# Kernel optimization log

Hardware: AMD Instinct MI355X
Metric: run time of the kernel (lower is better)

The kernel has to match this reference:

```python
import jax, jax.numpy as jnp
import numpy as np
import math

B, T, D, H = 4, 2048, 1024, 16
HD = D // H  # head dim = 64

def setup_inputs() -> dict:
    key = jax.random.key(0)
    ks = jax.random.split(key, 4)
    scale = 1.0 / math.sqrt(D)
    return {
        "x": jax.random.normal(ks[0], (B, T, D), dtype=jnp.float32),
        "Wq": jax.random.normal(ks[1], (D, D), dtype=jnp.float32) * scale,
        "bq": jnp.zeros((D,), dtype=jnp.float32),
        "Wk": jax.random.normal(ks[2], (D, D), dtype=jnp.float32) * scale,
        "bk": jnp.zeros((D,), dtype=jnp.float32),
        "Wv": jax.random.normal(ks[3], (D, D), dtype=jnp.float32) * scale,
        "bv": jnp.zeros((D,), dtype=jnp.float32),
    }

def reference(x, Wq, bq, Wk, bk, Wv, bv):
    b, t, d = x.shape
    # QKV projections (nn.Dense): x @ W + b
    q = x @ Wq + bq
    k = x @ Wk + bk
    v = x @ Wv + bv
    # b n (h d) -> b h n d
    def split_heads(y):
        return y.reshape(b, t, H, HD).transpose(0, 2, 1, 3)
    q, k, v = split_heads(q), split_heads(k), split_heads(v)
    # scaled dot-product attention; scale by sqrt(features // heads)
    scores = jnp.einsum("bhqd,bhkd->bhqk", q, k) / math.sqrt(HD)
    attn = jax.nn.softmax(scores, axis=-1)
    # dropout rate 0.0 / eval mode => identity
    out = jnp.einsum("bhqk,bhkd->bhqd", attn, v)
    # b h n d -> b n (h d)
    return out.transpose(0, 2, 1, 3).reshape(b, t, d)
```

## Files before the change

kernel.cpp:

```cpp
#include <hip/hip_runtime.h>
#include <math.h>

typedef unsigned short u16;
typedef short short8 __attribute__((ext_vector_type(8)));
typedef u16 u16x4 __attribute__((ext_vector_type(4)));
typedef float f32x4 __attribute__((ext_vector_type(4)));
typedef __bf16 bf16x8 __attribute__((ext_vector_type(8)));

#define B_ 4
#define T_ 2048
#define D_ 1024
#define H_ 16
#define HD_ 64
#define BT_ 8192

__device__ __forceinline__ u16 f2bf(float f) {
  unsigned u = __builtin_bit_cast(unsigned, f);
  u = u + 0x7fffu + ((u >> 16) & 1u);
  return (u16)(u >> 16);
}
__device__ __forceinline__ f32x4 mfma16(short8 a, short8 b, f32x4 c) {
  return __builtin_amdgcn_mfma_f32_16x16x32_bf16(
      __builtin_bit_cast(bf16x8, a), __builtin_bit_cast(bf16x8, b), c, 0, 0, 0);
}
__device__ __forceinline__ void async16(u16* lds, const u16* g) {
  __builtin_amdgcn_global_load_lds(
      (const __attribute__((address_space(1))) unsigned int*)g,
      (__attribute__((address_space(3))) unsigned int*)lds, 16, 0, 0);
}

__global__ __launch_bounds__(256) void convert_x(const float* __restrict__ in,
                                                 u16* __restrict__ out) {
  int i = (blockIdx.x * 256 + threadIdx.x) * 4;
  float4 v = *(const float4*)&in[i];
  u16x4 o = {f2bf(v.x), f2bf(v.y), f2bf(v.z), f2bf(v.w)};
  *(u16x4*)&out[i] = o;
}

__global__ __launch_bounds__(256) void transposeW3(
    const float* __restrict__ Wq, const float* __restrict__ Wk,
    const float* __restrict__ Wv, u16* __restrict__ wtq, u16* __restrict__ wtk,
    u16* __restrict__ wtv) {
  __shared__ float sh[32][33];
  const int wsel = blockIdx.y >> 5;
  const float* in = (wsel == 0) ? Wq : (wsel == 1) ? Wk : Wv;
  u16* out = (wsel == 0) ? wtq : (wsel == 1) ? wtk : wtv;
  const int bx = blockIdx.x * 32, by = (blockIdx.y & 31) * 32;
  const int col = threadIdx.x & 31, r8 = threadIdx.x >> 5;
#pragma unroll
  for (int i = 0; i < 4; i++) {
    int row = r8 + i * 8;
    sh[row][col] = in[(size_t)(by + row) * 1024 + bx + col];
  }
  __syncthreads();
#pragma unroll
  for (int i = 0; i < 4; i++) {
    int row = r8 + i * 8;
    out[(size_t)(bx + row) * 1024 + by + col] = f2bf(sh[col][row]);
  }
}

__global__ __launch_bounds__(256, 2) void gemm_qkv3(
    const u16* __restrict__ xbf, const u16* __restrict__ wtq,
    const u16* __restrict__ wtk, const u16* __restrict__ wtv,
    const float* __restrict__ bq, const float* __restrict__ bk,
    const float* __restrict__ bv, u16* __restrict__ qh, u16* __restrict__ kh,
    u16* __restrict__ vth, float qscale) {
  __shared__ __align__(16) u16 Rs[2][128 * 64];
  __shared__ __align__(16) u16 Cs[2][128 * 64];
  const int proj = blockIdx.y >> 3;
  const int fy = blockIdx.y & 7;
  const u16* Rm;
  const u16* Cm;
  const float* bias;
  u16* out;
  float scale;
  int r0, c0, vmode;
  if (proj == 0) {
    Rm = wtq; Cm = xbf; bias = bq; out = qh; scale = qscale; vmode = 0;
    r0 = fy * 128; c0 = blockIdx.x * 128;
  } else if (proj == 1) {
    Rm = wtk; Cm = xbf; bias = bk; out = kh; scale = 1.0f; vmode = 0;
    r0 = fy * 128; c0 = blockIdx.x * 128;
  } else {
    Rm = xbf; Cm = wtv; bias = bv; out = vth; scale = 1.0f; vmode = 1;
    r0 = blockIdx.x * 128; c0 = fy * 128;
  }
  const int tid = threadIdx.x;
  const int lane = tid & 63;
  const int w = tid >> 6;
  const int wr = w >> 1, wc = w & 1;
  const int c = lane & 15, q4 = lane >> 4;
  const int cx7 = c & 7;

  f32x4 acc[4][4];
#pragma unroll
  for (int i = 0; i < 4; i++)
#pragma unroll
    for (int j = 0; j < 4; j++) {
      f32x4 z = {0.f, 0.f, 0.f, 0.f};
      acc[i][j] = z;
    }

  const int sr = tid >> 3, pc = tid & 7;

#pragma unroll
  for (int i = 0; i < 4; i++) {
    int row = i * 32 + sr;
    int sc = (pc ^ (row & 7)) * 8;
    async16(&Rs[0][(i * 256 + tid) * 8], &Rm[(size_t)(r0 + row) * 1024 + sc]);
    async16(&Cs[0][(i * 256 + tid) * 8], &Cm[(size_t)(c0 + row) * 1024 + sc]);
  }

  for (int ks = 0; ks < 16; ks++) {
    const int cur = ks & 1;
    __syncthreads();
    if (ks + 1 < 16) {
      const int kk = (ks + 1) * 64;
#pragma unroll
      for (int i = 0; i < 4; i++) {
        int row = i * 32 + sr;
        int sc = (pc ^ (row & 7)) * 8;
        async16(&Rs[cur ^ 1][(i * 256 + tid) * 8],
                &Rm[(size_t)(r0 + row) * 1024 + kk + sc]);
        async16(&Cs[cur ^ 1][(i * 256 + tid) * 8],
                &Cm[(size_t)(c0 + row) * 1024 + kk + sc]);
      }
    }
#pragma unroll
    for (int h = 0; h < 2; h++) {
      short8 rF[4], cF[4];
      const int ko = ((h * 4 + q4) ^ cx7) * 8;
#pragma unroll
      for (int i = 0; i < 4; i++)
        rF[i] = *(const short8*)&Rs[cur][(wr * 64 + i * 16 + c) * 64 + ko];
#pragma unroll
      for (int j = 0; j < 4; j++)
        cF[j] = *(const short8*)&Cs[cur][(wc * 64 + j * 16 + c) * 64 + ko];
#pragma unroll
      for (int i = 0; i < 4; i++)
#pragma unroll
        for (int j = 0; j < 4; j++) acc[i][j] = mfma16(rF[i], cF[j], acc[i][j]);
    }
  }

  if (vmode == 0) {
#pragma unroll
    for (int i = 0; i < 4; i++) {
      int ng = r0 + wr * 64 + i * 16 + q4 * 4;
      int h = ng >> 6, hd = ng & 63;
#pragma unroll
      for (int j = 0; j < 4; j++) {
        int tg = c0 + wc * 64 + j * 16 + c;
        int b = tg >> 11, tt = tg & 2047;
        u16x4 o;
#pragma unroll
        for (int r = 0; r < 4; r++)
          o[r] = f2bf((acc[i][j][r] + bias[ng + r]) * scale);
        *(u16x4*)&out[(((size_t)(b * 16 + h) * 2048 + tt) << 6) + hd] = o;
      }
    }
  } else {
#pragma unroll
    for (int i = 0; i < 4; i++) {
      int tg = r0 + wr * 64 + i * 16 + q4 * 4;
      int b = tg >> 11, tt = tg & 2047;
      int tp = (tt & ~63) | (((tt >> 2) & 3) << 4) | (((tt >> 4) & 3) << 2);
#pragma unroll
      for (int j = 0; j < 4; j++) {
        int ng = c0 + wc * 64 + j * 16 + c;
        int h = ng >> 6, hd = ng & 63;
        float bb = bias[ng];
        u16x4 o;
#pragma unroll
        for (int r = 0; r < 4; r++) o[r] = f2bf(acc[i][j][r] + bb);
        *(u16x4*)&out[((size_t)((b * 16 + h) * 64 + hd)) * 2048 + tp] = o;
      }
    }
  }
}

__global__ __launch_bounds__(256, 2) void attn_fused(const u16* __restrict__ Qh,
                                                     const u16* __restrict__ Kh,
                                                     const u16* __restrict__ VTh,
                                                     float* __restrict__ out) {
  __shared__ __align__(16) u16 Ks[2][64 * 64];
  __shared__ __align__(16) u16 VTs[2][64 * 64];
  const int tid = threadIdx.x;
  const int w = tid >> 6, lane = tid & 63;
  const int c = lane & 15, q4 = lane >> 4;
  const int cx7 = c & 7;
  const int qt = blockIdx.x, bh = blockIdx.y;

  short8 qf[4][2];
#pragma unroll
  for (int nblk = 0; nblk < 4; nblk++) {
    const u16* Qp =
        Qh + ((size_t)bh * T_ + qt * 256 + w * 64 + nblk * 16 + c) * 64;
    qf[nblk][0] = *(const short8*)&Qp[q4 * 8];
    qf[nblk][1] = *(const short8*)&Qp[32 + q4 * 8];
  }

  const u16* Kb = Kh + (size_t)bh * T_ * 64;
  const u16* Vb = VTh + (size_t)bh * 64 * T_;

  f32x4 O[4][4];
#pragma unroll
  for (int nblk = 0; nblk < 4; nblk++)
#pragma unroll
    for (int nb = 0; nb < 4; nb++) {
      f32x4 z = {0.f, 0.f, 0.f, 0.f};
      O[nblk][nb] = z;
    }
  float lsum[4] = {0.f, 0.f, 0.f, 0.f};

  const int sr = tid >> 3, pc = tid & 7;

#pragma unroll
  for (int i = 0; i < 2; i++) {
    int r = i * 32 + sr;
    int sc = (pc ^ (r & 7)) * 8;
    async16(&Ks[0][(i * 256 + tid) * 8], &Kb[(size_t)r * 64 + sc]);
    async16(&VTs[0][(i * 256 + tid) * 8], &Vb[(size_t)r * T_ + sc]);
  }

  for (int it = 0; it < T_ / 64; it++) {
    const int cur = it & 1;
    __syncthreads();
    if (it + 1 < T_ / 64) {
      const int kt = (it + 1) * 64;
#pragma unroll
      for (int i = 0; i < 2; i++) {
        int r = i * 32 + sr;
        int sc = (pc ^ (r & 7)) * 8;
        async16(&Ks[cur ^ 1][(i * 256 + tid) * 8],
                &Kb[(size_t)(kt + r) * 64 + sc]);
        async16(&VTs[cur ^ 1][(i * 256 + tid) * 8],
                &Vb[(size_t)r * T_ + kt + sc]);
      }
    }

#pragma unroll
    for (int p = 0; p < 2; p++) {
      f32x4 S[2][4];
#pragma unroll
      for (int kbi = 0; kbi < 2; kbi++) {
        const int kb = p * 2 + kbi;
        short8 k0 =
            *(const short8*)&Ks[cur][(kb * 16 + c) * 64 + ((q4 ^ cx7) * 8)];
        short8 k1 = *(const short8*)&Ks[cur][(kb * 16 + c) * 64 +
                                             (((4 + q4) ^ cx7) * 8)];
#pragma unroll
        for (int nblk = 0; nblk < 4; nblk++) {
          f32x4 z = {0.f, 0.f, 0.f, 0.f};
          S[kbi][nblk] = mfma16(k0, qf[nblk][0], z);
          S[kbi][nblk] = mfma16(k1, qf[nblk][1], S[kbi][nblk]);
        }
      }

      short8 pf8[4];
#pragma unroll
      for (int nblk = 0; nblk < 4; nblk++) {
        float e[8];
#pragma unroll
        for (int kbi = 0; kbi < 2; kbi++)
#pragma unroll
          for (int r = 0; r < 4; r++)
            e[kbi * 4 + r] = __builtin_amdgcn_exp2f(S[kbi][nblk][r]);
        lsum[nblk] += ((e[0] + e[1]) + (e[2] + e[3])) +
                      ((e[4] + e[5]) + (e[6] + e[7]));
        bf16x8 t = {(__bf16)e[0], (__bf16)e[1], (__bf16)e[2], (__bf16)e[3],
                    (__bf16)e[4], (__bf16)e[5], (__bf16)e[6], (__bf16)e[7]};
        pf8[nblk] = __builtin_bit_cast(short8, t);
      }

#pragma unroll
      for (int nb = 0; nb < 4; nb++) {
        short8 vf = *(const short8*)&VTs[cur][(nb * 16 + c) * 64 +
                                              (((q4 * 2 + p) ^ cx7) * 8)];
#pragma unroll
        for (int nblk = 0; nblk < 4; nblk++)
          O[nblk][nb] = mfma16(pf8[nblk], vf, O[nblk][nb]);
      }
    }
  }

#pragma unroll
  for (int nblk = 0; nblk < 4; nblk++) {
    lsum[nblk] += __shfl_xor(lsum[nblk], 16);
    lsum[nblk] += __shfl_xor(lsum[nblk], 32);
  }

  const int bq = bh >> 4, h = bh & 15;
#pragma unroll
  for (int nblk = 0; nblk < 4; nblk++)
#pragma unroll
    for (int r = 0; r < 4; r++) {
      float rl = 1.0f / __shfl(lsum[nblk], q4 * 4 + r);
      int t = qt * 256 + w * 64 + nblk * 16 + q4 * 4 + r;
#pragma unroll
      for (int nb = 0; nb < 4; nb++)
        out[((size_t)(bq * T_ + t)) * 1024 + h * 64 + nb * 16 + c] =
            O[nblk][nb][r] * rl;
    }
}

extern "C" void kernel_launch(void* const* d_in, const int* in_sizes, int n_in,
                              void* d_out, int out_size, void* d_ws, size_t ws_size,
                              hipStream_t stream) {
  (void)in_sizes; (void)n_in; (void)out_size; (void)ws_size;
  const float* x  = (const float*)d_in[0];
  const float* Wq = (const float*)d_in[1];
  const float* bq = (const float*)d_in[2];
  const float* Wk = (const float*)d_in[3];
  const float* bk = (const float*)d_in[4];
  const float* Wv = (const float*)d_in[5];
  const float* bv = (const float*)d_in[6];
  float* out = (float*)d_out;

  u16* ob  = (u16*)d_out;
  u16* xbf = ob;
  u16* wtq = ob + (size_t)BT_ * D_;
  u16* wtk = wtq + (size_t)D_ * D_;
  u16* wtv = wtk + (size_t)D_ * D_;

  u16* ws  = (u16*)d_ws;
  u16* qh  = ws;
  u16* kh  = qh + (size_t)BT_ * D_;
  u16* vth = kh + (size_t)BT_ * D_;

  convert_x<<<8192, 256, 0, stream>>>(x, xbf);
  transposeW3<<<dim3(32, 96), 256, 0, stream>>>(Wq, Wk, Wv, wtq, wtk, wtv);

  const float qscale = 0.125f * 1.44269504088896f;
  gemm_qkv3<<<dim3(64, 24), 256, 0, stream>>>(xbf, wtq, wtk, wtv, bq, bk, bv,
                                              qh, kh, vth, qscale);

  attn_fused<<<dim3(8, 64), 256, 0, stream>>>(qh, kh, vth, out);
}
```

Measured before the change: 227.6 us.

## Merge prep kernels into one launch and deepen attention K/V pipeline to four buffers

The x conversion and weight transpose kernels are merged into a single launch, with blockIdx.y selecting which job a block does. This removes one kernel launch and lets both jobs run concurrently. The attention kernel moves from double to quad-buffered K/V tiles in LDS and processes two tiles per barrier, keeping more loads in flight and halving the number of __syncthreads. LDS use rises to 64KB per block, which may limit occupancy at two blocks per CU.

```diff
diff --git a/kernel.cpp b/kernel.cpp
--- a/kernel.cpp
+++ b/kernel.cpp
@@ -29,23 +29,25 @@
       (__attribute__((address_space(3))) unsigned int*)lds, 16, 0, 0);
 }
 
-__global__ __launch_bounds__(256) void convert_x(const float* __restrict__ in,
-                                                 u16* __restrict__ out) {
-  int i = (blockIdx.x * 256 + threadIdx.x) * 4;
-  float4 v = *(const float4*)&in[i];
-  u16x4 o = {f2bf(v.x), f2bf(v.y), f2bf(v.z), f2bf(v.w)};
-  *(u16x4*)&out[i] = o;
-}
-
-__global__ __launch_bounds__(256) void transposeW3(
-    const float* __restrict__ Wq, const float* __restrict__ Wk,
-    const float* __restrict__ Wv, u16* __restrict__ wtq, u16* __restrict__ wtk,
+__global__ __launch_bounds__(256) void prep(
+    const float* __restrict__ x, const float* __restrict__ Wq,
+    const float* __restrict__ Wk, const float* __restrict__ Wv,
+    u16* __restrict__ xbf, u16* __restrict__ wtq, u16* __restrict__ wtk,
     u16* __restrict__ wtv) {
   __shared__ float sh[32][33];
-  const int wsel = blockIdx.y >> 5;
+  if (blockIdx.y < 256) {
+    int bid = blockIdx.y * 32 + blockIdx.x;
+    int i = (bid * 256 + threadIdx.x) * 4;
+    float4 v = *(const float4*)&x[i];
+    u16x4 o = {f2bf(v.x), f2bf(v.y), f2bf(v.z), f2bf(v.w)};
+    *(u16x4*)&xbf[i] = o;
+    return;
+  }
+  const int yy = blockIdx.y - 256;
+  const int wsel = yy >> 5;
   const float* in = (wsel == 0) ? Wq : (wsel == 1) ? Wk : Wv;
   u16* out = (wsel == 0) ? wtq : (wsel == 1) ? wtk : wtv;
-  const int bx = blockIdx.x * 32, by = (blockIdx.y & 31) * 32;
+  const int bx = blockIdx.x * 32, by = (yy & 31) * 32;
   const int col = threadIdx.x & 31, r8 = threadIdx.x >> 5;
 #pragma unroll
   for (int i = 0; i < 4; i++) {
@@ -184,8 +186,8 @@
                                                      const u16* __restrict__ Kh,
                                                      const u16* __restrict__ VTh,
                                                      float* __restrict__ out) {
-  __shared__ __align__(16) u16 Ks[2][64 * 64];
-  __shared__ __align__(16) u16 VTs[2][64 * 64];
+  __shared__ __align__(16) u16 Ks[4][64 * 64];
+  __shared__ __align__(16) u16 VTs[4][64 * 64];
   const int tid = threadIdx.x;
   const int w = tid >> 6, lane = tid & 63;
   const int c = lane & 15, q4 = lane >> 4;
@@ -217,70 +219,79 @@
   const int sr = tid >> 3, pc = tid & 7;
 
 #pragma unroll
-  for (int i = 0; i < 2; i++) {
-    int r = i * 32 + sr;
-    int sc = (pc ^ (r & 7)) * 8;
-    async16(&Ks[0][(i * 256 + tid) * 8], &Kb[(size_t)r * 64 + sc]);
-    async16(&VTs[0][(i * 256 + tid) * 8], &Vb[(size_t)r * T_ + sc]);
-  }
-
-  for (int it = 0; it < T_ / 64; it++) {
-    const int cur = it & 1;
+  for (int tt = 0; tt < 2; tt++)
+#pragma unroll
+    for (int i = 0; i < 2; i++) {
+      int r = i * 32 + sr;
+      int sc = (pc ^ (r & 7)) * 8;
+      async16(&Ks[tt][(i * 256 + tid) * 8], &Kb[(size_t)(tt * 64 + r) * 64 + sc]);
+      async16(&VTs[tt][(i * 256 + tid) * 8], &Vb[(size_t)r * T_ + tt * 64 + sc]);
+    }
+
+  for (int it = 0; it < T_ / 64; it += 2) {
     __syncthreads();
-    if (it + 1 < T_ / 64) {
-      const int kt = (it + 1) * 64;
-#pragma unroll
-      for (int i = 0; i < 2; i++) {
-        int r = i * 32 + sr;
-        int sc = (pc ^ (r & 7)) * 8;
-        async16(&Ks[cur ^ 1][(i * 256 + tid) * 8],
-                &Kb[(size_t)(kt + r) * 64 + sc]);
-        async16(&VTs[cur ^ 1][(i * 256 + tid) * 8],
-                &Vb[(size_t)r * T_ + kt + sc]);
-      }
-    }
-
-#pragma unroll
-    for (int p = 0; p < 2; p++) {
-      f32x4 S[2][4];
-#pragma unroll
-      for (int kbi = 0; kbi < 2; kbi++) {
-        const int kb = p * 2 + kbi;
-        short8 k0 =
-            *(const short8*)&Ks[cur][(kb * 16 + c) * 64 + ((q4 ^ cx7) * 8)];
-        short8 k1 = *(const short8*)&Ks[cur][(kb * 16 + c) * 64 +
-                                             (((4 + q4) ^ cx7) * 8)];
+#pragma unroll
+    for (int tt = 2; tt < 4; tt++) {
+      if (it + tt < T_ / 64) {
+        const int kt = (it + tt) * 64;
+        const int buf = (it + tt) & 3;
+#pragma unroll
+        for (int i = 0; i < 2; i++) {
+          int r = i * 32 + sr;
+          int sc = (pc ^ (r & 7)) * 8;
+          async16(&Ks[buf][(i * 256 + tid) * 8],
+                  &Kb[(size_t)(kt + r) * 64 + sc]);
+          async16(&VTs[buf][(i * 256 + tid) * 8],
+                  &Vb[(size_t)r * T_ + kt + sc]);
+        }
+      }
+    }
+
+#pragma unroll
+    for (int tt = 0; tt < 2; tt++) {
+      const int cur = (it + tt) & 3;
+#pragma unroll
+      for (int p = 0; p < 2; p++) {
+        f32x4 S[2][4];
+#pragma unroll
+        for (int kbi = 0; kbi < 2; kbi++) {
+          const int kb = p * 2 + kbi;
+          short8 k0 =
+              *(const short8*)&Ks[cur][(kb * 16 + c) * 64 + ((q4 ^ cx7) * 8)];
+          short8 k1 = *(const short8*)&Ks[cur][(kb * 16 + c) * 64 +
+                                               (((4 + q4) ^ cx7) * 8)];
+#pragma unroll
+          for (int nblk = 0; nblk < 4; nblk++) {
+            f32x4 z = {0.f, 0.f, 0.f, 0.f};
+            S[kbi][nblk] = mfma16(k0, qf[nblk][0], z);
+            S[kbi][nblk] = mfma16(k1, qf[nblk][1], S[kbi][nblk]);
+          }
+        }
+
+        short8 pf8[4];
 #pragma unroll
         for (int nblk = 0; nblk < 4; nblk++) {
-          f32x4 z = {0.f, 0.f, 0.f, 0.f};
-          S[kbi][nblk] = mfma16(k0, qf[nblk][0], z);
-          S[kbi][nblk] = mfma16(k1, qf[nblk][1], S[kbi][nblk]);
+          float e[8];
+#pragma unroll
+          for (int kbi = 0; kbi < 2; kbi++)
+#pragma unroll
+            for (int r = 0; r < 4; r++)
+              e[kbi * 4 + r] = __builtin_amdgcn_exp2f(S[kbi][nblk][r]);
+          lsum[nblk] += ((e[0] + e[1]) + (e[2] + e[3])) +
+                        ((e[4] + e[5]) + (e[6] + e[7]));
+          bf16x8 t = {(__bf16)e[0], (__bf16)e[1], (__bf16)e[2], (__bf16)e[3],
+                      (__bf16)e[4], (__bf16)e[5], (__bf16)e[6], (__bf16)e[7]};
+          pf8[nblk] = __builtin_bit_cast(short8, t);
         }
-      }
-
-      short8 pf8[4];
-#pragma unroll
-      for (int nblk = 0; nblk < 4; nblk++) {
-        float e[8];
-#pragma unroll
-        for (int kbi = 0; kbi < 2; kbi++)
-#pragma unroll
-          for (int r = 0; r < 4; r++)
-            e[kbi * 4 + r] = __builtin_amdgcn_exp2f(S[kbi][nblk][r]);
-        lsum[nblk] += ((e[0] + e[1]) + (e[2] + e[3])) +
-                      ((e[4] + e[5]) + (e[6] + e[7]));
-        bf16x8 t = {(__bf16)e[0], (__bf16)e[1], (__bf16)e[2], (__bf16)e[3],
-                    (__bf16)e[4], (__bf16)e[5], (__bf16)e[6], (__bf16)e[7]};
-        pf8[nblk] = __builtin_bit_cast(short8, t);
-      }
-
-#pragma unroll
-      for (int nb = 0; nb < 4; nb++) {
-        short8 vf = *(const short8*)&VTs[cur][(nb * 16 + c) * 64 +
-                                              (((q4 * 2 + p) ^ cx7) * 8)];
-#pragma unroll
-        for (int nblk = 0; nblk < 4; nblk++)
-          O[nblk][nb] = mfma16(pf8[nblk], vf, O[nblk][nb]);
+
+#pragma unroll
+        for (int nb = 0; nb < 4; nb++) {
+          short8 vf = *(const short8*)&VTs[cur][(nb * 16 + c) * 64 +
+                                                (((q4 * 2 + p) ^ cx7) * 8)];
+#pragma unroll
+          for (int nblk = 0; nblk < 4; nblk++)
+            O[nblk][nb] = mfma16(pf8[nblk], vf, O[nblk][nb]);
+        }
       }
     }
   }
@@ -329,8 +340,7 @@
   u16* kh  = qh + (size_t)BT_ * D_;
   u16* vth = kh + (size_t)BT_ * D_;
 
-  convert_x<<<8192, 256, 0, stream>>>(x, xbf);
-  transposeW3<<<dim3(32, 96), 256, 0, stream>>>(Wq, Wk, Wv, wtq, wtk, wtv);
+  prep<<<dim3(32, 352), 256, 0, stream>>>(x, Wq, Wk, Wv, xbf, wtq, wtk, wtv);
 
   const float qscale = 0.125f * 1.44269504088896f;
   gemm_qkv3<<<dim3(64, 24), 256, 0, stream>>>(xbf, wtq, wtk, wtv, bq, bk, bv,
```

New measurement: 277.3 us. +21.8%, slower.
